# Kernel optimization log

Measured on AMD Instinct MI355X. Metric: run time of the kernel, lower is better.

## Reference

```python
import jax, jax.numpy as jnp
import numpy as np

B, S, D = 64, 2048, 512

def setup_inputs() -> dict:
    key = jax.random.key(0)
    ks = jax.random.split(key, 7)
    return {
        "sent_vec": jax.random.normal(ks[0], (B, S, D), dtype=jnp.float32),
        "c1_vec": jax.random.normal(ks[1], (B, D), dtype=jnp.float32),
        "c2_vec": jax.random.normal(ks[2], (B, D), dtype=jnp.float32),
        "c3_vec": jax.random.normal(ks[3], (B, D), dtype=jnp.float32),
        "c4_vec": jax.random.normal(ks[4], (B, D), dtype=jnp.float32),
        "kernel": jax.random.normal(ks[5], (D, D), dtype=jnp.float32) * 0.05,
        "bias": jax.random.normal(ks[6], (D, 1), dtype=jnp.float32) * 0.05,
    }

def reference(sent_vec, c1_vec, c2_vec, c3_vec, c4_vec, kernel, bias):
    # Wh: [B,S,D], bh: [B,S]
    Wh = jnp.einsum("bsd,de->bse", sent_vec, kernel)
    bh = jnp.einsum("bsd,do->bs", sent_vec, bias)  # bias is [D,1]
    c = jnp.stack([c1_vec, c2_vec, c3_vec, c4_vec], axis=0)  # [4,B,D]
    # scores: [4,B,S] = Wh . u + bh, softmax over seq axis
    scores = jnp.einsum("bse,cbe->cbs", Wh, c) + bh[None]
    attn = jax.nn.softmax(scores, axis=-1)
    # weighted sum over seq: [4,B,D]
    P = jnp.einsum("cbs,bsd->cbd", attn, sent_vec)
    return (P[0], P[1], P[2], P[3])
```

## Files before the change

### kernel.cpp

```cpp
#include <hip/hip_runtime.h>
#include <hip/hip_bf16.h>
#include <math.h>

constexpr int B = 64;
constexpr int S = 2048;
constexpr int D = 512;
constexpr int NCHUNK = 8;
constexpr int CHUNK = S / NCHUNK;
constexpr int NW = 4;
constexpr int ROWS_PER_WAVE = CHUNK / NW;
constexpr int NGRP = ROWS_PER_WAVE / 4;
constexpr int NPART = NCHUNK * NW;

__global__ __launch_bounds__(256) void compute_v_kernel(
    const float* __restrict__ K, const float* __restrict__ bias,
    const float* __restrict__ c1, const float* __restrict__ c2,
    const float* __restrict__ c3, const float* __restrict__ c4,
    float* __restrict__ v)
{
    const int b = blockIdx.y;
    const int dchunk = blockIdx.x;
    __shared__ float c_lds[4][D];

    const float* cptr0 = c1 + (size_t)b * D;
    const float* cptr1 = c2 + (size_t)b * D;
    const float* cptr2 = c3 + (size_t)b * D;
    const float* cptr3 = c4 + (size_t)b * D;
    for (int i = threadIdx.x; i < D; i += 256) {
        c_lds[0][i] = cptr0[i];
        c_lds[1][i] = cptr1[i];
        c_lds[2][i] = cptr2[i];
        c_lds[3][i] = cptr3[i];
    }
    __syncthreads();

    const int wave = threadIdx.x >> 6;
    const int lane = threadIdx.x & 63;

    #pragma unroll
    for (int r = 0; r < 16; ++r) {
        const int d = dchunk * 64 + wave * 16 + r;
        const float* krow = K + (size_t)d * D;
        float a0 = 0.f, a1 = 0.f, a2 = 0.f, a3 = 0.f;
        #pragma unroll
        for (int k = 0; k < D / 64; ++k) {
            const float kv = krow[k * 64 + lane];
            a0 = fmaf(kv, c_lds[0][k * 64 + lane], a0);
            a1 = fmaf(kv, c_lds[1][k * 64 + lane], a1);
            a2 = fmaf(kv, c_lds[2][k * 64 + lane], a2);
            a3 = fmaf(kv, c_lds[3][k * 64 + lane], a3);
        }
        #pragma unroll
        for (int off = 32; off; off >>= 1) {
            a0 += __shfl_xor(a0, off);
            a1 += __shfl_xor(a1, off);
            a2 += __shfl_xor(a2, off);
            a3 += __shfl_xor(a3, off);
        }
        if (lane == 0) {
            const float bv = bias[d];
            v[((size_t)0 * B + b) * D + d] = a0 + bv;
            v[((size_t)1 * B + b) * D + d] = a1 + bv;
            v[((size_t)2 * B + b) * D + d] = a2 + bv;
            v[((size_t)3 * B + b) * D + d] = a3 + bv;
        }
    }
}

__global__ __launch_bounds__(256) void flash_kernel(
    const float* __restrict__ sent, const float* __restrict__ v,
    float* __restrict__ partML, float* __restrict__ partP)
{
    const int b = blockIdx.y;
    const int ch = blockIdx.x;
    const int t = threadIdx.x;
    const int wave = t >> 6;
    const int lane = t & 63;

    float vlo[4][4], vhi[4][4];
    #pragma unroll
    for (int c = 0; c < 4; ++c) {
        const float4 lo = *(const float4*)&v[((size_t)c * B + b) * D + lane * 4];
        const float4 hi = *(const float4*)&v[((size_t)c * B + b) * D + 256 + lane * 4];
        vlo[c][0] = lo.x; vlo[c][1] = lo.y; vlo[c][2] = lo.z; vlo[c][3] = lo.w;
        vhi[c][0] = hi.x; vhi[c][1] = hi.y; vhi[c][2] = hi.z; vhi[c][3] = hi.w;
    }

    const size_t sbase = ((size_t)b * S + (size_t)ch * CHUNK + (size_t)wave * ROWS_PER_WAVE) * D;

    float m = -INFINITY, lsum = 0.f;
    float plo[4][4] = {{0}}, phi[4][4] = {{0}};

    float xA[4][8], xB[4][8];

    auto loadg = [&](float (&x)[4][8], int g) {
        const float* src = sent + sbase + (size_t)g * 4 * D + lane * 4;
        #pragma unroll
        for (int rr = 0; rr < 4; ++rr) {
            const float4 lo = *(const float4*)(src + rr * D);
            const float4 hi = *(const float4*)(src + rr * D + 256);
            x[rr][0] = lo.x; x[rr][1] = lo.y; x[rr][2] = lo.z; x[rr][3] = lo.w;
            x[rr][4] = hi.x; x[rr][5] = hi.y; x[rr][6] = hi.z; x[rr][7] = hi.w;
        }
    };

    auto compute = [&](float (&x)[4][8]) {
        float s[4];
        #pragma unroll
        for (int rr = 0; rr < 4; ++rr) {
            float a0 = 0.f, a1 = 0.f, a2 = 0.f, a3 = 0.f;
            #pragma unroll
            for (int j = 0; j < 4; ++j) {
                a0 = fmaf(x[rr][j], vlo[0][j], a0); a0 = fmaf(x[rr][4 + j], vhi[0][j], a0);
                a1 = fmaf(x[rr][j], vlo[1][j], a1); a1 = fmaf(x[rr][4 + j], vhi[1][j], a1);
                a2 = fmaf(x[rr][j], vlo[2][j], a2); a2 = fmaf(x[rr][4 + j], vhi[2][j], a2);
                a3 = fmaf(x[rr][j], vlo[3][j], a3); a3 = fmaf(x[rr][4 + j], vhi[3][j], a3);
            }
            float u  = (lane & 1) ? a1 : a0;
            float uo = (lane & 1) ? a0 : a1;
            u += __shfl_xor(uo, 1);
            float w_ = (lane & 1) ? a3 : a2;
            float wo = (lane & 1) ? a2 : a3;
            w_ += __shfl_xor(wo, 1);
            float p  = (lane & 2) ? w_ : u;
            float q  = (lane & 2) ? u : w_;
            p += __shfl_xor(q, 2);
            p += __shfl_xor(p, 4);
            p += __shfl_xor(p, 8);
            p += __shfl_xor(p, 16);
            p += __shfl_xor(p, 32);
            s[rr] = p;
        }

        const float tm = fmaxf(fmaxf(s[0], s[1]), fmaxf(s[2], s[3]));
        const float mn = fmaxf(m, tm);
        const float cr = __expf(m - mn);
        m = mn;
        lsum *= cr;
        float w4[4];
        #pragma unroll
        for (int rr = 0; rr < 4; ++rr) { w4[rr] = __expf(s[rr] - mn); lsum += w4[rr]; }

        #pragma unroll
        for (int c = 0; c < 4; ++c) {
            const float crc = __int_as_float(__builtin_amdgcn_readlane(__float_as_int(cr), c));
            #pragma unroll
            for (int j = 0; j < 4; ++j) { plo[c][j] *= crc; phi[c][j] *= crc; }
        }
        #pragma unroll
        for (int rr = 0; rr < 4; ++rr) {
            #pragma unroll
            for (int c = 0; c < 4; ++c) {
                const float wc = __int_as_float(__builtin_amdgcn_readlane(__float_as_int(w4[rr]), c));
                plo[c][0] = fmaf(wc, x[rr][0], plo[c][0]);
                plo[c][1] = fmaf(wc, x[rr][1], plo[c][1]);
                plo[c][2] = fmaf(wc, x[rr][2], plo[c][2]);
                plo[c][3] = fmaf(wc, x[rr][3], plo[c][3]);
                phi[c][0] = fmaf(wc, x[rr][4], phi[c][0]);
                phi[c][1] = fmaf(wc, x[rr][5], phi[c][1]);
                phi[c][2] = fmaf(wc, x[rr][6], phi[c][2]);
                phi[c][3] = fmaf(wc, x[rr][7], phi[c][3]);
            }
        }
    };

    loadg(xA, 0);
    for (int g = 0; g < NGRP; g += 2) {
        loadg(xB, g + 1);
        compute(xA);
        if (g + 2 < NGRP) loadg(xA, g + 2);
        compute(xB);
    }

    const int pi = (b * NCHUNK + ch) * NW + wave;
    #pragma unroll
    for (int c = 0; c < 4; ++c) {
        const float4 lo4 = make_float4(plo[c][0], plo[c][1], plo[c][2], plo[c][3]);
        const float4 hi4 = make_float4(phi[c][0], phi[c][1], phi[c][2], phi[c][3]);
        *(float4*)&partP[((size_t)pi * 4 + c) * D + lane * 4] = lo4;
        *(float4*)&partP[((size_t)pi * 4 + c) * D + 256 + lane * 4] = hi4;
    }
    if (lane < 4) {
        partML[(pi * 4 + lane) * 2 + 0] = m;
        partML[(pi * 4 + lane) * 2 + 1] = lsum;
    }
}

__global__ __launch_bounds__(128) void combine_kernel(
    const float* __restrict__ partML, const float* __restrict__ partP,
    float* __restrict__ out)
{
    const int c = blockIdx.x & 3;
    const int b = blockIdx.x >> 2;
    const int t = threadIdx.x;
    const int base_pi = b * NPART;

    float mg = -INFINITY;
    for (int i = 0; i < NPART; ++i)
        mg = fmaxf(mg, partML[((base_pi + i) * 4 + c) * 2 + 0]);

    float lg = 0.f;
    float4 acc = make_float4(0.f, 0.f, 0.f, 0.f);
    for (int i = 0; i < NPART; ++i) {
        const float mi = partML[((base_pi + i) * 4 + c) * 2 + 0];
        const float li = partML[((base_pi + i) * 4 + c) * 2 + 1];
        const float sc = __expf(mi - mg);
        lg += sc * li;
        const float4 p = *(const float4*)&partP[((size_t)(base_pi + i) * 4 + c) * D + t * 4];
        acc.x = fmaf(sc, p.x, acc.x);
        acc.y = fmaf(sc, p.y, acc.y);
        acc.z = fmaf(sc, p.z, acc.z);
        acc.w = fmaf(sc, p.w, acc.w);
    }
    const float inv = 1.f / lg;
    acc.x *= inv; acc.y *= inv; acc.z *= inv; acc.w *= inv;
    *(float4*)&out[((size_t)c * B + b) * D + t * 4] = acc;
}

extern "C" void kernel_launch(void* const* d_in, const int* in_sizes, int n_in,
                              void* d_out, int out_size, void* d_ws, size_t ws_size,
                              hipStream_t stream)
{
    const float* sent = (const float*)d_in[0];
    const float* c1   = (const float*)d_in[1];
    const float* c2   = (const float*)d_in[2];
    const float* c3   = (const float*)d_in[3];
    const float* c4   = (const float*)d_in[4];
    const float* K    = (const float*)d_in[5];
    const float* bias = (const float*)d_in[6];
    float* out = (float*)d_out;

    float* v      = (float*)d_ws;
    float* partML = (float*)((char*)d_ws + 4 * B * D * 4);
    float* partP  = (float*)((char*)d_ws + 4 * B * D * 4
                             + B * NPART * 4 * 2 * 4);

    compute_v_kernel<<<dim3(8, B), 256, 0, stream>>>(K, bias, c1, c2, c3, c4, v);
    flash_kernel<<<dim3(NCHUNK, B), 256, 0, stream>>>(sent, v, partML, partP);
    combine_kernel<<<4 * B, 128, 0, stream>>>(partML, partP, out);
}
```

Before: 74.80 us.

## Merge per-wave softmax partials in LDS and skip redundant rescaling

The flash kernel now merges its four waves' partial accumulators in shared memory before writing to global, so global partials shrink fourfold and the combine kernel reads 8 partials instead of 32. The online-softmax rescale now runs only when some lane's running max increases, decided wave-wide with __all. The v-computation reduction uses a transpose-style shuffle so four results share one reduction chain. This adds 32KB of LDS per block and a block-wide sync, which could lower occupancy.

```diff
diff --git a/kernel.cpp b/kernel.cpp
--- a/kernel.cpp
+++ b/kernel.cpp
@@ -10,7 +10,7 @@
 constexpr int NW = 4;
 constexpr int ROWS_PER_WAVE = CHUNK / NW;
 constexpr int NGRP = ROWS_PER_WAVE / 4;
-constexpr int NPART = NCHUNK * NW;
+constexpr int NPART = NCHUNK;
 
 __global__ __launch_bounds__(256) void compute_v_kernel(
     const float* __restrict__ K, const float* __restrict__ bias,
@@ -50,20 +50,21 @@
             a2 = fmaf(kv, c_lds[2][k * 64 + lane], a2);
             a3 = fmaf(kv, c_lds[3][k * 64 + lane], a3);
         }
-        #pragma unroll
-        for (int off = 32; off; off >>= 1) {
-            a0 += __shfl_xor(a0, off);
-            a1 += __shfl_xor(a1, off);
-            a2 += __shfl_xor(a2, off);
-            a3 += __shfl_xor(a3, off);
-        }
-        if (lane == 0) {
-            const float bv = bias[d];
-            v[((size_t)0 * B + b) * D + d] = a0 + bv;
-            v[((size_t)1 * B + b) * D + d] = a1 + bv;
-            v[((size_t)2 * B + b) * D + d] = a2 + bv;
-            v[((size_t)3 * B + b) * D + d] = a3 + bv;
-        }
+        float u  = (lane & 1) ? a1 : a0;
+        float uo = (lane & 1) ? a0 : a1;
+        u += __shfl_xor(uo, 1);
+        float w_ = (lane & 1) ? a3 : a2;
+        float wo = (lane & 1) ? a2 : a3;
+        w_ += __shfl_xor(wo, 1);
+        float p  = (lane & 2) ? w_ : u;
+        float q  = (lane & 2) ? u : w_;
+        p += __shfl_xor(q, 2);
+        p += __shfl_xor(p, 4);
+        p += __shfl_xor(p, 8);
+        p += __shfl_xor(p, 16);
+        p += __shfl_xor(p, 32);
+        if (lane < 4)
+            v[((size_t)lane * B + b) * D + d] = p + bias[d];
     }
 }
 
@@ -76,6 +77,9 @@
     const int t = threadIdx.x;
     const int wave = t >> 6;
     const int lane = t & 63;
+
+    __shared__ float p_lds[NW][4][D];
+    __shared__ float ml_lds[NW][4][2];
 
     float vlo[4][4], vhi[4][4];
     #pragma unroll
@@ -133,20 +137,22 @@
         }
 
         const float tm = fmaxf(fmaxf(s[0], s[1]), fmaxf(s[2], s[3]));
-        const float mn = fmaxf(m, tm);
-        const float cr = __expf(m - mn);
-        m = mn;
-        lsum *= cr;
+        if (!__all(tm <= m)) {
+            const float mn = fmaxf(m, tm);
+            const float cr = __expf(m - mn);
+            m = mn;
+            lsum *= cr;
+            #pragma unroll
+            for (int c = 0; c < 4; ++c) {
+                const float crc = __int_as_float(__builtin_amdgcn_readlane(__float_as_int(cr), c));
+                #pragma unroll
+                for (int j = 0; j < 4; ++j) { plo[c][j] *= crc; phi[c][j] *= crc; }
+            }
+        }
         float w4[4];
         #pragma unroll
-        for (int rr = 0; rr < 4; ++rr) { w4[rr] = __expf(s[rr] - mn); lsum += w4[rr]; }
-
-        #pragma unroll
-        for (int c = 0; c < 4; ++c) {
-            const float crc = __int_as_float(__builtin_amdgcn_readlane(__float_as_int(cr), c));
-            #pragma unroll
-            for (int j = 0; j < 4; ++j) { plo[c][j] *= crc; phi[c][j] *= crc; }
-        }
+        for (int rr = 0; rr < 4; ++rr) { w4[rr] = __expf(s[rr] - m); lsum += w4[rr]; }
+
         #pragma unroll
         for (int rr = 0; rr < 4; ++rr) {
             #pragma unroll
@@ -172,17 +178,55 @@
         compute(xB);
     }
 
-    const int pi = (b * NCHUNK + ch) * NW + wave;
     #pragma unroll
     for (int c = 0; c < 4; ++c) {
-        const float4 lo4 = make_float4(plo[c][0], plo[c][1], plo[c][2], plo[c][3]);
-        const float4 hi4 = make_float4(phi[c][0], phi[c][1], phi[c][2], phi[c][3]);
-        *(float4*)&partP[((size_t)pi * 4 + c) * D + lane * 4] = lo4;
-        *(float4*)&partP[((size_t)pi * 4 + c) * D + 256 + lane * 4] = hi4;
-    }
-    if (lane < 4) {
-        partML[(pi * 4 + lane) * 2 + 0] = m;
-        partML[(pi * 4 + lane) * 2 + 1] = lsum;
+        *(float4*)&p_lds[wave][c][lane * 4] =
+            make_float4(plo[c][0], plo[c][1], plo[c][2], plo[c][3]);
+        *(float4*)&p_lds[wave][c][256 + lane * 4] =
+            make_float4(phi[c][0], phi[c][1], phi[c][2], phi[c][3]);
+    }
+    if (lane < 4) { ml_lds[wave][lane][0] = m; ml_lds[wave][lane][1] = lsum; }
+    __syncthreads();
+
+    {
+        const int c = wave;
+        float mi0 = ml_lds[0][c][0], mi1 = ml_lds[1][c][0];
+        float mi2 = ml_lds[2][c][0], mi3 = ml_lds[3][c][0];
+        const float mg = fmaxf(fmaxf(mi0, mi1), fmaxf(mi2, mi3));
+        const float e0 = __expf(mi0 - mg), e1 = __expf(mi1 - mg);
+        const float e2 = __expf(mi2 - mg), e3 = __expf(mi3 - mg);
+        const float lg = e0 * ml_lds[0][c][1] + e1 * ml_lds[1][c][1]
+                       + e2 * ml_lds[2][c][1] + e3 * ml_lds[3][c][1];
+
+        float4 aLo = make_float4(0.f, 0.f, 0.f, 0.f);
+        float4 aHi = make_float4(0.f, 0.f, 0.f, 0.f);
+        const float ee[1] = {0};  (void)ee;
+        {
+            const float4 q0 = *(const float4*)&p_lds[0][c][lane * 4];
+            const float4 q1 = *(const float4*)&p_lds[1][c][lane * 4];
+            const float4 q2 = *(const float4*)&p_lds[2][c][lane * 4];
+            const float4 q3 = *(const float4*)&p_lds[3][c][lane * 4];
+            aLo.x = e0*q0.x + e1*q1.x + e2*q2.x + e3*q3.x;
+            aLo.y = e0*q0.y + e1*q1.y + e2*q2.y + e3*q3.y;
+            aLo.z = e0*q0.z + e1*q1.z + e2*q2.z + e3*q3.z;
+            aLo.w = e0*q0.w + e1*q1.w + e2*q2.w + e3*q3.w;
+            const float4 r0 = *(const float4*)&p_lds[0][c][256 + lane * 4];
+            const float4 r1 = *(const float4*)&p_lds[1][c][256 + lane * 4];
+            const float4 r2 = *(const float4*)&p_lds[2][c][256 + lane * 4];
+            const float4 r3 = *(const float4*)&p_lds[3][c][256 + lane * 4];
+            aHi.x = e0*r0.x + e1*r1.x + e2*r2.x + e3*r3.x;
+            aHi.y = e0*r0.y + e1*r1.y + e2*r2.y + e3*r3.y;
+            aHi.z = e0*r0.z + e1*r1.z + e2*r2.z + e3*r3.z;
+            aHi.w = e0*r0.w + e1*r1.w + e2*r2.w + e3*r3.w;
+        }
+
+        const size_t pb = (size_t)(b * NCHUNK + ch) * 4 + c;
+        *(float4*)&partP[pb * D + lane * 4] = aLo;
+        *(float4*)&partP[pb * D + 256 + lane * 4] = aHi;
+        if (lane == 0) {
+            partML[pb * 2 + 0] = mg;
+            partML[pb * 2 + 1] = lg;
+        }
     }
 }
 
@@ -193,20 +237,22 @@
     const int c = blockIdx.x & 3;
     const int b = blockIdx.x >> 2;
     const int t = threadIdx.x;
-    const int base_pi = b * NPART;
 
     float mg = -INFINITY;
+    #pragma unroll
     for (int i = 0; i < NPART; ++i)
-        mg = fmaxf(mg, partML[((base_pi + i) * 4 + c) * 2 + 0]);
+        mg = fmaxf(mg, partML[((size_t)(b * NCHUNK + i) * 4 + c) * 2 + 0]);
 
     float lg = 0.f;
     float4 acc = make_float4(0.f, 0.f, 0.f, 0.f);
+    #pragma unroll
     for (int i = 0; i < NPART; ++i) {
-        const float mi = partML[((base_pi + i) * 4 + c) * 2 + 0];
-        const float li = partML[((base_pi + i) * 4 + c) * 2 + 1];
+        const size_t pb = (size_t)(b * NCHUNK + i) * 4 + c;
+        const float mi = partML[pb * 2 + 0];
+        const float li = partML[pb * 2 + 1];
         const float sc = __expf(mi - mg);
         lg += sc * li;
-        const float4 p = *(const float4*)&partP[((size_t)(base_pi + i) * 4 + c) * D + t * 4];
+        const float4 p = *(const float4*)&partP[pb * D + t * 4];
         acc.x = fmaf(sc, p.x, acc.x);
         acc.y = fmaf(sc, p.y, acc.y);
         acc.z = fmaf(sc, p.z, acc.z);
@@ -233,7 +279,7 @@
     float* v      = (float*)d_ws;
     float* partML = (float*)((char*)d_ws + 4 * B * D * 4);
     float* partP  = (float*)((char*)d_ws + 4 * B * D * 4
-                             + B * NPART * 4 * 2 * 4);
+                             + B * NCHUNK * 4 * 2 * 4);
 
     compute_v_kernel<<<dim3(8, B), 256, 0, stream>>>(K, bias, c1, c2, c3, c4, v);
     flash_kernel<<<dim3(NCHUNK, B), 256, 0, stream>>>(sent, v, partML, partP);
```

Result: faster. 67.25 us (-10.1%).
